# Kernel optimization log

Measured on AMD Instinct MI355X. Metric: run time of the kernel, lower is better.

Reference implementation:

```python
import jax, jax.numpy as jnp
import numpy as np

B, S, N, F, H, E, L = 16, 64, 128, 16, 64, 1024, 2
NEG_SLOPE = 0.2


def _gat_layer(h, src, tgt, Wl, bl, Wr, br, att, bo):
    # h: [B,S,N,H]; src/tgt: [Et] (edges incl. self-loops)
    xl = jnp.einsum('bsnf,hf->bsnh', h, Wl) + bl
    xr = jnp.einsum('bsnf,hf->bsnh', h, Wr) + br
    e = xl[:, :, src] + xr[:, :, tgt]                       # [B,S,Et,H]
    e = jnp.where(e > 0, e, NEG_SLOPE * e)                  # leaky_relu(0.2)
    a = jnp.einsum('bseh,h->bse', e, att)                   # [B,S,Et]
    # segment softmax over target node (stable)
    m = jnp.full(a.shape[:2] + (N,), -jnp.inf, a.dtype).at[:, :, tgt].max(a)
    p = jnp.exp(a - m[:, :, tgt])
    z = jnp.zeros(a.shape[:2] + (N,), a.dtype).at[:, :, tgt].add(p)
    alpha = p / z[:, :, tgt]
    out = jnp.zeros_like(xl).at[:, :, tgt].add(alpha[..., None] * xl[:, :, src])
    return out + bo


def _forward(x, edge_index, in_W, in_b, gat_Wl, gat_bl, gat_Wr, gat_br,
             gat_att, gat_bias, gru_Wih, gru_Whh, gru_bih, gru_bhh,
             oh_W1, oh_b1, oh_W2, oh_b2, dh_W1, dh_b1, dh_W2, dh_b2):
    ar = jnp.arange(N, dtype=edge_index.dtype)
    ei = jnp.concatenate([edge_index, jnp.stack([ar, ar])], axis=1)  # add self-loops
    src, tgt = ei[0], ei[1]
    h = jnp.einsum('bsnf,hf->bsnh', x, in_W) + in_b          # input_proj
    for l in range(L):
        h = jax.nn.relu(_gat_layer(h, src, tgt, gat_Wl[l], gat_bl[l],
                                   gat_Wr[l], gat_br[l], gat_att[l], gat_bias[l]))
    # [B,S,N,H] -> sequences [B*N, S, H]; GRU, keep last state
    seqs = h.transpose(0, 2, 1, 3).reshape(B * N, S, H)

    def step(hprev, xt):
        gi = xt @ gru_Wih.T + gru_bih
        gh = hprev @ gru_Whh.T + gru_bhh
        ir, iz, inn = jnp.split(gi, 3, axis=-1)
        hr, hz, hn = jnp.split(gh, 3, axis=-1)
        r = jax.nn.sigmoid(ir + hr)
        zz = jax.nn.sigmoid(iz + hz)
        n = jnp.tanh(inn + r * hn)
        hnew = (1 - zz) * n + zz * hprev
        return hnew, None

    h0 = jnp.zeros((B * N, H), h.dtype)
    h_last, _ = jax.lax.scan(step, h0, seqs.transpose(1, 0, 2))
    h_last = h_last.reshape(B, N, H)

    def head(hh, W1, b1, W2, b2):
        return jax.nn.relu(hh @ W1.T + b1) @ W2.T + b2

    order = head(h_last, oh_W1, oh_b1, oh_W2, oh_b2)        # [B,N,1]
    demand = head(h_last, dh_W1, dh_b1, dh_W2, dh_b2)       # [B,N,1]
    return order, demand


def setup_inputs() -> dict:
    key = jax.random.key(0)
    ks = jax.random.split(key, 16)
    def g(i, shp, s=0.05):
        return (jax.random.normal(ks[i], shp) * s).astype(jnp.float32)
    x = jax.random.normal(ks[0], (B, S, N, F), dtype=jnp.float32)
    src = jax.random.randint(ks[1], (E,), 0, N)
    off = jax.random.randint(ks[2], (E,), 1, N)
    edge_index = jnp.stack([src, (src + off) % N]).astype(jnp.int32)  # no self-loops
    zf = lambda shp: jnp.zeros(shp, jnp.float32)
    return dict(
        x=x, edge_index=edge_index,
        in_W=g(3, (H, F)), in_b=zf((H,)),
        gat_Wl=g(4, (L, H, H)), gat_bl=zf((L, H)),
        gat_Wr=g(5, (L, H, H)), gat_br=zf((L, H)),
        gat_att=g(6, (L, H), 0.1), gat_bias=zf((L, H)),
        gru_Wih=g(7, (3 * H, H)), gru_Whh=g(8, (3 * H, H)),
        gru_bih=zf((3 * H,)), gru_bhh=zf((3 * H,)),
        oh_W1=g(9, (H // 2, H)), oh_b1=zf((H // 2,)),
        oh_W2=g(10, (1, H // 2)), oh_b2=zf((1,)),
        dh_W1=g(11, (H // 2, H)), dh_b1=zf((H // 2,)),
        dh_W2=g(12, (1, H // 2)), dh_b2=zf((1,)),
    )


def reference(x, edge_index, in_W, in_b, gat_Wl, gat_bl, gat_Wr, gat_br,
              gat_att, gat_bias, gru_Wih, gru_Whh, gru_bih, gru_bhh,
              oh_W1, oh_b1, oh_W2, oh_b2, dh_W1, dh_b1, dh_W2, dh_b2):
    return _forward(x, edge_index, in_W, in_b, gat_Wl, gat_bl, gat_Wr, gat_br,
                    gat_att, gat_bias, gru_Wih, gru_Whh, gru_bih, gru_bhh,
                    oh_W1, oh_b1, oh_W2, oh_b2, dh_W1, dh_b1, dh_W2, dh_b2)
```

## Files before the change

### kernel.cpp

```cpp
#include <hip/hip_runtime.h>
#include <math.h>

#define BB 16
#define SS 64
#define NN 128
#define FF 16
#define HH 64
#define EE 1024
#define ET 1152
#define LLAYERS 2
#define XPAD 65
#define RT (BB * SS * NN)

__device__ __forceinline__ float readlane_f(float v, int k) {
  return __int_as_float(__builtin_amdgcn_readlane(__float_as_int(v), k));
}
__device__ __forceinline__ unsigned flipf(float f) {
  unsigned u = __float_as_uint(f);
  unsigned mask = (u & 0x80000000u) ? 0xFFFFFFFFu : 0x80000000u;
  return u ^ mask;
}
__device__ __forceinline__ float unflipf(unsigned u) {
  unsigned b = (u & 0x80000000u) ? (u ^ 0x80000000u) : ~u;
  return __uint_as_float(b);
}
__device__ __forceinline__ float sigmoidf_(float x) { return 1.f / (1.f + expf(-x)); }

__global__ void setup_csr_kernel(const int* __restrict__ ei,
                                 int* __restrict__ off,
                                 int* __restrict__ csrc,
                                 int* __restrict__ ctgt) {
  __shared__ int deg[NN], cur[NN], offs[NN + 1];
  int tid = threadIdx.x;
  if (tid < NN) deg[tid] = 0;
  __syncthreads();
  for (int e = tid; e < ET; e += 256) {
    int tg = (e < EE) ? ei[EE + e] : (e - EE);
    atomicAdd(&deg[tg], 1);
  }
  __syncthreads();
  if (tid == 0) {
    int s = 0;
    for (int i = 0; i < NN; ++i) { offs[i] = s; s += deg[i]; }
    offs[NN] = s;
  }
  __syncthreads();
  if (tid < NN) cur[tid] = offs[tid];
  if (tid <= NN) off[tid] = offs[tid];
  __syncthreads();
  for (int e = tid; e < ET; e += 256) {
    int sv, tg;
    if (e < EE) { sv = ei[e]; tg = ei[EE + e]; }
    else        { sv = e - EE; tg = e - EE; }
    int pos = atomicAdd(&cur[tg], 1);
    csrc[pos] = sv;
    ctgt[pos] = tg;
  }
}

__global__ __launch_bounds__(256) void input_proj_kernel(
    const float* __restrict__ x, const float* __restrict__ W,
    const float* __restrict__ bvec, float* __restrict__ h) {
  int lane = threadIdx.x & 63;
  int wid = threadIdx.x >> 6;
  float wreg[FF];
#pragma unroll
  for (int i = 0; i < FF / 4; ++i)
    *(float4*)&wreg[4 * i] = ((const float4*)(W + lane * FF))[i];
  float bias = bvec[lane];
  int row0 = __builtin_amdgcn_readfirstlane((blockIdx.x * 4 + wid) * 32);
#pragma unroll 2
  for (int r = 0; r < 32; ++r) {
    int row = row0 + r;
    const float* xr = x + row * FF;
    float acc = bias;
#pragma unroll
    for (int f = 0; f < FF; ++f) acc += xr[f] * wreg[f];
    h[row * HH + lane] = acc;
  }
}

__global__ __launch_bounds__(128) void xlxr_kernel(
    const float* __restrict__ hin,
    const float* __restrict__ Wl, const float* __restrict__ bl,
    const float* __restrict__ Wr, const float* __restrict__ br,
    float* __restrict__ xl, float* __restrict__ xr) {
  __shared__ float lsh[64 * 68];
  int tid = threadIdx.x;
  int j = tid & 63;
  int w = tid >> 6;
  int row0 = blockIdx.x * 64;
  {
    const float4* src4 = (const float4*)(hin + (size_t)row0 * HH);
#pragma unroll
    for (int i = 0; i < 8; ++i) {
      int idx = i * 128 + tid;
      int r = idx >> 4, c = idx & 15;
      *(float4*)&lsh[r * 68 + c * 4] = src4[idx];
    }
  }
  const float* W  = w ? Wr : Wl;
  const float* bv = w ? br : bl;
  float* outp     = w ? xr : xl;
  float wreg[HH];
  {
    const float4* ws_ = (const float4*)(W + (size_t)j * HH);
#pragma unroll
    for (int i = 0; i < HH / 4; ++i) *(float4*)&wreg[4 * i] = ws_[i];
  }
  float bias = bv[j];
  int rloc = j & 31;
  __syncthreads();

#pragma unroll 1
  for (int b = 0; b < 2; ++b) {
    float hreg[32];
    {
      const float* hr = &lsh[(b * 32 + rloc) * 68 + 32];
#pragma unroll
      for (int i = 0; i < 8; ++i)
        *(float4*)&hreg[4 * i] = *(const float4*)&hr[4 * i];
    }
#pragma unroll 1
    for (int r = 0; r < 32; ++r) {
      const float* hrow = &lsh[(b * 32 + r) * 68];
      float a0 = bias, a1 = 0.f, a2 = 0.f, a3 = 0.f;
#pragma unroll
      for (int k = 0; k < 32; k += 4) {
        float4 hb = *(const float4*)&hrow[k];
        a0 += hb.x * wreg[k + 0];
        a1 += hb.y * wreg[k + 1];
        a2 += hb.z * wreg[k + 2];
        a3 += hb.w * wreg[k + 3];
      }
#pragma unroll
      for (int q = 0; q < 32; q += 4) {
        a0 += readlane_f(hreg[q + 0], r) * wreg[32 + q + 0];
        a1 += readlane_f(hreg[q + 1], r) * wreg[32 + q + 1];
        a2 += readlane_f(hreg[q + 2], r) * wreg[32 + q + 2];
        a3 += readlane_f(hreg[q + 3], r) * wreg[32 + q + 3];
      }
      outp[(size_t)(row0 + b * 32 + r) * HH + j] = (a0 + a1) + (a2 + a3);
    }
  }
}

__global__ __launch_bounds__(256) void gat_edge_kernel(
    const float* __restrict__ xl_g, const float* __restrict__ xr_g,
    float* __restrict__ hout,
    const int* __restrict__ csr_off, const int* __restrict__ csr_src,
    const int* __restrict__ csr_tgt,
    const float* __restrict__ att, const float* __restrict__ bo) {
  __shared__ float xl_sh[NN * XPAD];
  __shared__ float xr_sh[NN * XPAD];
  __shared__ float p_sh[ET];
  __shared__ int st_sh[ET];
  __shared__ unsigned m_sh[NN];
  int tid = threadIdx.x, lane = tid & 63, wid = tid >> 6;
  int base = blockIdx.x * (NN * HH);

#pragma unroll 1
  for (int i = tid * 4; i < NN * HH; i += 256 * 4) {
    int row = i >> 6, h = i & 63;
    float4 vl = *(const float4*)(xl_g + base + i);
    float4 vr = *(const float4*)(xr_g + base + i);
    float* dl = xl_sh + row * XPAD + h;
    float* dr = xr_sh + row * XPAD + h;
    dl[0] = vl.x; dl[1] = vl.y; dl[2] = vl.z; dl[3] = vl.w;
    dr[0] = vr.x; dr[1] = vr.y; dr[2] = vr.z; dr[3] = vr.w;
  }
  for (int i = tid; i < ET; i += 256)
    st_sh[i] = csr_src[i] | (csr_tgt[i] << 16);
  if (tid < NN) m_sh[tid] = 0u;
  __syncthreads();

#pragma unroll 1
  for (int e = tid; e < ET; e += 256) {
    int st = st_sh[e];
    int s = st & 0xffff, tg = st >> 16;
    const float* xlr = xl_sh + s * XPAD;
    const float* xrr = xr_sh + tg * XPAD;
    float a0 = 0.f, a1 = 0.f, a2 = 0.f, a3 = 0.f;
#pragma unroll
    for (int h = 0; h < HH; h += 4) {
      float v0 = xlr[h + 0] + xrr[h + 0]; v0 = (v0 > 0.f) ? v0 : 0.2f * v0;
      float v1 = xlr[h + 1] + xrr[h + 1]; v1 = (v1 > 0.f) ? v1 : 0.2f * v1;
      float v2 = xlr[h + 2] + xrr[h + 2]; v2 = (v2 > 0.f) ? v2 : 0.2f * v2;
      float v3 = xlr[h + 3] + xrr[h + 3]; v3 = (v3 > 0.f) ? v3 : 0.2f * v3;
      a0 += v0 * att[h + 0];
      a1 += v1 * att[h + 1];
      a2 += v2 * att[h + 2];
      a3 += v3 * att[h + 3];
    }
    float a = (a0 + a1) + (a2 + a3);
    p_sh[e] = a;
    atomicMax(&m_sh[tg], flipf(a));
  }
  __syncthreads();

  for (int e = tid; e < ET; e += 256) {
    int tg = st_sh[e] >> 16;
    p_sh[e] = expf(p_sh[e] - unflipf(m_sh[tg]));
  }
  __syncthreads();

  float bo_l = bo[lane];
#pragma unroll 1
  for (int n = wid; n < NN; n += 4) {
    int o0 = __builtin_amdgcn_readfirstlane(csr_off[n]);
    int o1 = __builtin_amdgcn_readfirstlane(csr_off[n + 1]);
    float acc = 0.f, z = 0.f;
    for (int i = o0; i < o1; ++i) {
      float p = p_sh[i];
      int s = st_sh[i] & 0xffff;
      acc += p * xl_sh[s * XPAD + lane];
      z += p;
    }
    float o = acc / z + bo_l;
    hout[base + n * HH + lane] = fmaxf(o, 0.f);
  }
}

__device__ __forceinline__ void gemm_half(
    const float* __restrict__ hin, int base,
    const float* __restrict__ W, const float* __restrict__ bvec,
    float* __restrict__ out_sh, int half, int lane) {
  float wreg[HH];
#pragma unroll
  for (int i = 0; i < HH / 4; ++i)
    *(float4*)&wreg[4 * i] = ((const float4*)(W + lane * HH))[i];
  float bias = bvec[lane];
  int n0 = __builtin_amdgcn_readfirstlane(half * 64);
#pragma unroll 1
  for (int nd = 0; nd < 64; ++nd) {
    int node = n0 + nd;
    const float* hrow = hin + base + node * HH;
    float a0 = bias, a1 = 0.f, a2 = 0.f, a3 = 0.f;
#pragma unroll
    for (int f = 0; f < HH; f += 4) {
      a0 += hrow[f + 0] * wreg[f + 0];
      a1 += hrow[f + 1] * wreg[f + 1];
      a2 += hrow[f + 2] * wreg[f + 2];
      a3 += hrow[f + 3] * wreg[f + 3];
    }
    out_sh[node * HH + lane] = (a0 + a1) + (a2 + a3);
  }
}

__global__ __launch_bounds__(256) void gat_fused_kernel(
    const float* __restrict__ hin, float* __restrict__ hout,
    const int* __restrict__ csr_off, const int* __restrict__ csr_src,
    const int* __restrict__ csr_tgt,
    const float* __restrict__ Wl, const float* __restrict__ bl,
    const float* __restrict__ Wr, const float* __restrict__ br,
    const float* __restrict__ att, const float* __restrict__ bo) {
  __shared__ float xl_sh[NN * HH];
  __shared__ float xr_sh[NN * HH];
  __shared__ float p_sh[ET];
  __shared__ int st_sh[ET];
  __shared__ unsigned m_sh[NN];
  int tid = threadIdx.x, lane = tid & 63, wid = tid >> 6;
  int base = blockIdx.x * (NN * HH);

  for (int i = tid; i < ET; i += 256)
    st_sh[i] = csr_src[i] | (csr_tgt[i] << 16);
  if (tid < NN) m_sh[tid] = 0u;

  if (wid < 2) gemm_half(hin, base, Wl, bl, xl_sh, wid & 1, lane);
  else         gemm_half(hin, base, Wr, br, xr_sh, wid & 1, lane);

  float att_l = att[lane];
  float bo_l = bo[lane];
  __syncthreads();

#pragma unroll 1
  for (int e = wid; e < ET; e += 4) {
    int st = st_sh[e];
    int s = st & 0xffff, tg = st >> 16;
    float v = xl_sh[s * HH + lane] + xr_sh[tg * HH + lane];
    v = (v > 0.f) ? v : 0.2f * v;
    float prod = v * att_l;
#pragma unroll
    for (int mm = 32; mm; mm >>= 1) prod += __shfl_xor(prod, mm);
    if (lane == 0) {
      p_sh[e] = prod;
      atomicMax(&m_sh[tg], flipf(prod));
    }
  }
  __syncthreads();

  for (int e = tid; e < ET; e += 256) {
    int tg = st_sh[e] >> 16;
    p_sh[e] = expf(p_sh[e] - unflipf(m_sh[tg]));
  }
  __syncthreads();

#pragma unroll 1
  for (int n = wid; n < NN; n += 4) {
    int o0 = csr_off[n], o1 = csr_off[n + 1];
    float acc = 0.f, z = 0.f;
    for (int i = o0; i < o1; ++i) {
      float p = p_sh[i];
      int s = st_sh[i] & 0xffff;
      acc += p * xl_sh[s * HH + lane];
      z += p;
    }
    float o = acc / z + bo_l;
    hout[base + n * HH + lane] = fmaxf(o, 0.f);
  }
}

__global__ __launch_bounds__(192) void gi_proj_kernel(
    const float* __restrict__ hin, const float* __restrict__ Wih,
    const float* __restrict__ bih, float* __restrict__ gi) {
  __shared__ float lsh[64 * 68];
  int tid = threadIdx.x;
  int j = tid & 63;
  int g = tid >> 6;
  int row0 = blockIdx.x * 64;
  {
    const float4* src4 = (const float4*)(hin + (size_t)row0 * HH);
#pragma unroll 1
    for (int i = tid; i < 1024; i += 192) {
      int r = i >> 4, c = i & 15;
      *(float4*)&lsh[r * 68 + c * 4] = src4[i];
    }
  }
  float wreg[HH];
  {
    const float4* ws_ = (const float4*)(Wih + (size_t)(g * 64 + j) * HH);
#pragma unroll
    for (int i = 0; i < HH / 4; ++i) *(float4*)&wreg[4 * i] = ws_[i];
  }
  float bias = bih[g * 64 + j];
  int rloc = j & 31;
  __syncthreads();

#pragma unroll 1
  for (int b = 0; b < 2; ++b) {
    float hreg[32];
    {
      const float* hr = &lsh[(b * 32 + rloc) * 68 + 32];
#pragma unroll
      for (int i = 0; i < 8; ++i)
        *(float4*)&hreg[4 * i] = *(const float4*)&hr[4 * i];
    }
#pragma unroll 1
    for (int r = 0; r < 32; ++r) {
      const float* hrow = &lsh[(b * 32 + r) * 68];
      float a0 = bias, a1 = 0.f, a2 = 0.f, a3 = 0.f;
#pragma unroll
      for (int k = 0; k < 32; k += 4) {
        float4 hb = *(const float4*)&hrow[k];
        a0 += hb.x * wreg[k + 0];
        a1 += hb.y * wreg[k + 1];
        a2 += hb.z * wreg[k + 2];
        a3 += hb.w * wreg[k + 3];
      }
#pragma unroll
      for (int q = 0; q < 32; q += 4) {
        a0 += readlane_f(hreg[q + 0], r) * wreg[32 + q + 0];
        a1 += readlane_f(hreg[q + 1], r) * wreg[32 + q + 1];
        a2 += readlane_f(hreg[q + 2], r) * wreg[32 + q + 2];
        a3 += readlane_f(hreg[q + 3], r) * wreg[32 + q + 3];
      }
      gi[(size_t)(row0 + b * 32 + r) * 192 + g * 64 + j] = (a0 + a1) + (a2 + a3);
    }
  }
}

__global__ __launch_bounds__(64, 2) void gru_rec_kernel(
    const float* __restrict__ gi,
    const float* __restrict__ Whh, const float* __restrict__ bhh,
    const float* __restrict__ oW1, const float* __restrict__ ob1,
    const float* __restrict__ oW2, const float* __restrict__ ob2,
    const float* __restrict__ dW1, const float* __restrict__ db1,
    const float* __restrict__ dW2, const float* __restrict__ db2,
    float* __restrict__ out) {
  int lane = threadIdx.x;
  int seq = blockIdx.x;
  int b = seq >> 7, n = seq & (NN - 1);

  float wr[HH], wz[HH], wn[HH];
  {
    const float4* s0 = (const float4*)(Whh + (size_t)(0 * 64 + lane) * HH);
    const float4* s1 = (const float4*)(Whh + (size_t)(1 * 64 + lane) * HH);
    const float4* s2 = (const float4*)(Whh + (size_t)(2 * 64 + lane) * HH);
#pragma unroll
    for (int i = 0; i < HH / 4; ++i) {
      *(float4*)&wr[4 * i] = s0[i];
      *(float4*)&wz[4 * i] = s1[i];
      *(float4*)&wn[4 * i] = s2[i];
    }
  }
  float br_ = bhh[lane], bz_ = bhh[64 + lane], bn_ = bhh[128 + lane];

  const float* gbase = gi + ((size_t)b * SS * NN + (size_t)n) * 192;
  float gir = gbase[lane], giz = gbase[64 + lane], gin = gbase[128 + lane];
  const float* g1 = gbase + (size_t)NN * 192;
  float pir = g1[lane], piz = g1[64 + lane], pin = g1[128 + lane];
  float hj = 0.f;

#pragma unroll 1
  for (int t = 0; t < SS; ++t) {
    float qir = 0.f, qiz = 0.f, qin = 0.f;
    if (t + 2 < SS) {
      const float* g2 = gbase + (size_t)(t + 2) * NN * 192;
      qir = g2[lane]; qiz = g2[64 + lane]; qin = g2[128 + lane];
    }
    float ar0 = br_, ar1 = 0.f, az0 = bz_, az1 = 0.f, an0 = bn_, an1 = 0.f;
#pragma unroll
    for (int k = 0; k < HH; k += 2) {
      float h0 = readlane_f(hj, k), h1 = readlane_f(hj, k + 1);
      ar0 += h0 * wr[k];     az0 += h0 * wz[k];     an0 += h0 * wn[k];
      ar1 += h1 * wr[k + 1]; az1 += h1 * wz[k + 1]; an1 += h1 * wn[k + 1];
    }
    float r  = sigmoidf_(gir + ar0 + ar1);
    float z  = sigmoidf_(giz + az0 + az1);
    float nn_ = tanhf(gin + r * (an0 + an1));
    hj = (1.f - z) * nn_ + z * hj;
    gir = pir; giz = piz; gin = pin;
    pir = qir; piz = qiz; pin = qin;
  }

  int half = lane >> 5, jp = lane & 31;
  const float* W1 = half ? dW1 : oW1;
  const float* b1 = half ? db1 : ob1;
  const float* W2 = half ? dW2 : oW2;
  const float* b2 = half ? db2 : ob2;
  float wv[HH];
#pragma unroll
  for (int i = 0; i < HH / 4; ++i)
    *(float4*)&wv[4 * i] = ((const float4*)(W1 + jp * HH))[i];
  float acc = b1[jp];
#pragma unroll
  for (int k = 0; k < HH; ++k)
    acc += readlane_f(hj, k) * wv[k];
  float val = fmaxf(acc, 0.f) * W2[jp];
  val += __shfl_down(val, 16, 32);
  val += __shfl_down(val, 8, 32);
  val += __shfl_down(val, 4, 32);
  val += __shfl_down(val, 2, 32);
  val += __shfl_down(val, 1, 32);
  if (jp == 0) out[half * (BB * NN) + seq] = val + b2[0];
}

__global__ __launch_bounds__(192, 3) void gru_fused_kernel(
    const float* __restrict__ hbuf,
    const float* __restrict__ Wih, const float* __restrict__ Whh,
    const float* __restrict__ bih, const float* __restrict__ bhh,
    const float* __restrict__ oW1, const float* __restrict__ ob1,
    const float* __restrict__ oW2, const float* __restrict__ ob2,
    const float* __restrict__ dW1, const float* __restrict__ db1,
    const float* __restrict__ dW2, const float* __restrict__ db2,
    float* __restrict__ out) {
  __shared__ float gi_sh[SS * 3 * HH];
  __shared__ float exch[2][3][HH];

  int lane = threadIdx.x & 63;
  int g = (int)threadIdx.x >> 6;
  int seq = blockIdx.x;
  int b = seq >> 7, n = seq & (NN - 1);
  const float* xbase = hbuf + ((size_t)b * SS * NN + (size_t)n) * HH;

  {
    float w[HH];
    const float4* wsrc = (const float4*)(Wih + (size_t)(g * 64 + lane) * HH);
#pragma unroll
    for (int i = 0; i < HH / 4; ++i) *(float4*)&w[4 * i] = wsrc[i];
    float bias = bih[g * 64 + lane];
#pragma unroll 2
    for (int t = 0; t < SS; ++t) {
      const float* xr = xbase + (size_t)t * NN * HH;
      float a0 = bias, a1 = 0.f, a2 = 0.f, a3 = 0.f;
#pragma unroll
      for (int k = 0; k < HH; k += 4) {
        float4 xb = *(const float4*)(xr + k);
        a0 += xb.x * w[k + 0];
        a1 += xb.y * w[k + 1];
        a2 += xb.z * w[k + 2];
        a3 += xb.w * w[k + 3];
      }
      gi_sh[(t * 3 + g) * HH + lane] = (a0 + a1) + (a2 + a3);
    }
  }

  float whh[HH];
  {
    const float4* wsrc = (const float4*)(Whh + (size_t)(g * 64 + lane) * HH);
#pragma unroll
    for (int i = 0; i < HH / 4; ++i) *(float4*)&whh[4 * i] = wsrc[i];
  }
  float bhg = bhh[g * 64 + lane];
  float hj = 0.f;
  __syncthreads();

#pragma unroll 1
  for (int t = 0; t < SS; ++t) {
    float a0 = bhg, a1 = 0.f, a2 = 0.f, a3 = 0.f;
#pragma unroll
    for (int k = 0; k < HH; k += 4) {
      a0 += readlane_f(hj, k + 0) * whh[k + 0];
      a1 += readlane_f(hj, k + 1) * whh[k + 1];
      a2 += readlane_f(hj, k + 2) * whh[k + 2];
      a3 += readlane_f(hj, k + 3) * whh[k + 3];
    }
    float gh = (a0 + a1) + (a2 + a3);
    int slot = t & 1;
    exch[slot][g][lane] = gh;
    __syncthreads();
    float ghr = exch[slot][0][lane];
    float ghz = exch[slot][1][lane];
    float ghn = exch[slot][2][lane];
    float gir = gi_sh[(t * 3 + 0) * HH + lane];
    float giz = gi_sh[(t * 3 + 1) * HH + lane];
    float gin = gi_sh[(t * 3 + 2) * HH + lane];
    float r  = sigmoidf_(gir + ghr);
    float z  = sigmoidf_(giz + ghz);
    float nn_ = tanhf(gin + r * ghn);
    hj = (1.f - z) * nn_ + z * hj;
  }

  if (g == 0) {
    int half = lane >> 5, jp = lane & 31;
    const float* W1 = half ? dW1 : oW1;
    const float* b1 = half ? db1 : ob1;
    const float* W2 = half ? dW2 : oW2;
    const float* b2 = half ? db2 : ob2;
    float wv[HH];
#pragma unroll
    for (int i = 0; i < HH / 4; ++i)
      *(float4*)&wv[4 * i] = ((const float4*)(W1 + jp * HH))[i];
    float acc = b1[jp];
#pragma unroll
    for (int k = 0; k < HH; ++k)
      acc += readlane_f(hj, k) * wv[k];
    float val = fmaxf(acc, 0.f) * W2[jp];
    val += __shfl_down(val, 16, 32);
    val += __shfl_down(val, 8, 32);
    val += __shfl_down(val, 4, 32);
    val += __shfl_down(val, 2, 32);
    val += __shfl_down(val, 1, 32);
    if (jp == 0) out[half * (BB * NN) + seq] = val + b2[0];
  }
}

extern "C" void kernel_launch(void* const* d_in, const int* in_sizes, int n_in,
                              void* d_out, int out_size, void* d_ws, size_t ws_size,
                              hipStream_t stream) {
  const float* x       = (const float*)d_in[0];
  const int*   ei      = (const int*)d_in[1];
  const float* in_W    = (const float*)d_in[2];
  const float* in_b    = (const float*)d_in[3];
  const float* gat_Wl  = (const float*)d_in[4];
  const float* gat_bl  = (const float*)d_in[5];
  const float* gat_Wr  = (const float*)d_in[6];
  const float* gat_br  = (const float*)d_in[7];
  const float* gat_att = (const float*)d_in[8];
  const float* gat_bias= (const float*)d_in[9];
  const float* gru_Wih = (const float*)d_in[10];
  const float* gru_Whh = (const float*)d_in[11];
  const float* gru_bih = (const float*)d_in[12];
  const float* gru_bhh = (const float*)d_in[13];
  const float* oh_W1   = (const float*)d_in[14];
  const float* oh_b1   = (const float*)d_in[15];
  const float* oh_W2   = (const float*)d_in[16];
  const float* oh_b2   = (const float*)d_in[17];
  const float* dh_W1   = (const float*)d_in[18];
  const float* dh_b1   = (const float*)d_in[19];
  const float* dh_W2   = (const float*)d_in[20];
  const float* dh_b2   = (const float*)d_in[21];
  float* out = (float*)d_out;

  char* ws = (char*)d_ws;
  size_t hfloats = (size_t)BB * SS * NN * HH;
  float* hbuf = (float*)ws;
  size_t off_csr = hfloats * sizeof(float);
  size_t off_buf = off_csr + (160 + 2 * ET) * sizeof(int);
  off_buf = (off_buf + 255) & ~(size_t)255;
  int* csr_off = (int*)(ws + off_csr);
  int* csr_src = csr_off + 160;
  int* csr_tgt = csr_src + ET;
  float* xlbuf = (float*)(ws + off_buf);
  float* xrbuf = xlbuf + hfloats;
  size_t need_gat = off_buf + 2 * hfloats * sizeof(float);
  bool big_gat = (ws_size >= need_gat);
  float* gibuf = (float*)(ws + off_buf);
  size_t need_gru = off_buf + (size_t)RT * 192 * sizeof(float);
  bool big_gru = (ws_size >= need_gru);

  setup_csr_kernel<<<1, 256, 0, stream>>>(ei, csr_off, csr_src, csr_tgt);
  input_proj_kernel<<<(BB * SS * NN) / (4 * 32), 256, 0, stream>>>(x, in_W, in_b, hbuf);
  for (int l = 0; l < LLAYERS; ++l) {
    if (big_gat) {
      xlxr_kernel<<<RT / 64, 128, 0, stream>>>(
          hbuf, gat_Wl + l * HH * HH, gat_bl + l * HH,
          gat_Wr + l * HH * HH, gat_br + l * HH, xlbuf, xrbuf);
      gat_edge_kernel<<<BB * SS, 256, 0, stream>>>(
          xlbuf, xrbuf, hbuf, csr_off, csr_src, csr_tgt,
          gat_att + l * HH, gat_bias + l * HH);
    } else {
      gat_fused_kernel<<<BB * SS, 256, 0, stream>>>(
          hbuf, hbuf, csr_off, csr_src, csr_tgt,
          gat_Wl + l * HH * HH, gat_bl + l * HH,
          gat_Wr + l * HH * HH, gat_br + l * HH,
          gat_att + l * HH, gat_bias + l * HH);
    }
  }
  if (big_gru) {
    gi_proj_kernel<<<RT / 64, 192, 0, stream>>>(hbuf, gru_Wih, gru_bih, gibuf);
    gru_rec_kernel<<<BB * NN, 64, 0, stream>>>(
        gibuf, gru_Whh, gru_bhh,
        oh_W1, oh_b1, oh_W2, oh_b2, dh_W1, dh_b1, dh_W2, dh_b2, out);
  } else {
    gru_fused_kernel<<<BB * NN, 192, 0, stream>>>(
        hbuf, gru_Wih, gru_Whh, gru_bih, gru_bhh,
        oh_W1, oh_b1, oh_W2, oh_b2, dh_W1, dh_b1, dh_W2, dh_b2, out);
  }
}
```

Baseline: 632.1 us.

## Fuse GAT xl/xr projection into edge kernel with shared-memory staging

Replaces the separate xl/xr projection kernel and edge-softmax kernel with one 512-thread kernel per (batch, step) slice. The h slice is staged in LDS, the projections are computed straight into LDS, and then the attention and aggregation run from there. This removes the global write and read of the xl/xr buffers, which are twice the size of h, plus one launch per layer. The cost is a heavier LDS footprint per block, which may limit occupancy. The old fallback path for a small workspace is also removed.

```diff
diff --git a/kernel.cpp b/kernel.cpp
--- a/kernel.cpp
+++ b/kernel.cpp
@@ -10,6 +10,7 @@
 #define ET 1152
 #define LLAYERS 2
 #define XPAD 65
+#define HSTRIDE 68
 #define RT (BB * SS * NN)
 
 __device__ __forceinline__ float readlane_f(float v, int k) {
@@ -80,50 +81,59 @@
   }
 }
 
-__global__ __launch_bounds__(128) void xlxr_kernel(
-    const float* __restrict__ hin,
+__global__ __launch_bounds__(512) void gat_fused2_kernel(
+    float* __restrict__ hio,
+    const int* __restrict__ csr_off, const int* __restrict__ csr_src,
+    const int* __restrict__ csr_tgt,
     const float* __restrict__ Wl, const float* __restrict__ bl,
     const float* __restrict__ Wr, const float* __restrict__ br,
-    float* __restrict__ xl, float* __restrict__ xr) {
-  __shared__ float lsh[64 * 68];
-  int tid = threadIdx.x;
-  int j = tid & 63;
-  int w = tid >> 6;
-  int row0 = blockIdx.x * 64;
-  {
-    const float4* src4 = (const float4*)(hin + (size_t)row0 * HH);
-#pragma unroll
-    for (int i = 0; i < 8; ++i) {
-      int idx = i * 128 + tid;
+    const float* __restrict__ att, const float* __restrict__ bo) {
+  __shared__ float h_sh[NN * HSTRIDE];
+  __shared__ float xl_sh[NN * XPAD];
+  __shared__ float xr_sh[NN * XPAD];
+  __shared__ float p_sh[ET];
+  __shared__ int st_sh[ET];
+  __shared__ unsigned m_sh[NN];
+  int tid = threadIdx.x, lane = tid & 63, wid = tid >> 6;
+  int base = blockIdx.x * (NN * HH);
+
+  {
+    const float4* src4 = (const float4*)(hio + base);
+#pragma unroll
+    for (int i = 0; i < 4; ++i) {
+      int idx = i * 512 + tid;
       int r = idx >> 4, c = idx & 15;
-      *(float4*)&lsh[r * 68 + c * 4] = src4[idx];
-    }
-  }
-  const float* W  = w ? Wr : Wl;
-  const float* bv = w ? br : bl;
-  float* outp     = w ? xr : xl;
-  float wreg[HH];
-  {
-    const float4* ws_ = (const float4*)(W + (size_t)j * HH);
-#pragma unroll
-    for (int i = 0; i < HH / 4; ++i) *(float4*)&wreg[4 * i] = ws_[i];
-  }
-  float bias = bv[j];
-  int rloc = j & 31;
-  __syncthreads();
-
-#pragma unroll 1
-  for (int b = 0; b < 2; ++b) {
+      *(float4*)&h_sh[r * HSTRIDE + c * 4] = src4[idx];
+    }
+  }
+  for (int i = tid; i < ET; i += 512)
+    st_sh[i] = csr_src[i] | (csr_tgt[i] << 16);
+  if (tid < NN) m_sh[tid] = 0u;
+  __syncthreads();
+
+  {
+    int mat = wid >> 2;
+    const float* W  = mat ? Wr : Wl;
+    const float* bv = mat ? br : bl;
+    float* outsh    = mat ? xr_sh : xl_sh;
+    float wreg[HH];
+    {
+      const float4* ws_ = (const float4*)(W + (size_t)lane * HH);
+#pragma unroll
+      for (int i = 0; i < HH / 4; ++i) *(float4*)&wreg[4 * i] = ws_[i];
+    }
+    float bias = bv[lane];
+    int r0 = (wid & 3) * 32;
     float hreg[32];
     {
-      const float* hr = &lsh[(b * 32 + rloc) * 68 + 32];
+      const float* hr = &h_sh[(r0 + (lane & 31)) * HSTRIDE + 32];
 #pragma unroll
       for (int i = 0; i < 8; ++i)
         *(float4*)&hreg[4 * i] = *(const float4*)&hr[4 * i];
     }
 #pragma unroll 1
     for (int r = 0; r < 32; ++r) {
-      const float* hrow = &lsh[(b * 32 + r) * 68];
+      const float* hrow = &h_sh[(r0 + r) * HSTRIDE];
       float a0 = bias, a1 = 0.f, a2 = 0.f, a3 = 0.f;
 #pragma unroll
       for (int k = 0; k < 32; k += 4) {
@@ -140,42 +150,13 @@
         a2 += readlane_f(hreg[q + 2], r) * wreg[32 + q + 2];
         a3 += readlane_f(hreg[q + 3], r) * wreg[32 + q + 3];
       }
-      outp[(size_t)(row0 + b * 32 + r) * HH + j] = (a0 + a1) + (a2 + a3);
-    }
-  }
-}
-
-__global__ __launch_bounds__(256) void gat_edge_kernel(
-    const float* __restrict__ xl_g, const float* __restrict__ xr_g,
-    float* __restrict__ hout,
-    const int* __restrict__ csr_off, const int* __restrict__ csr_src,
-    const int* __restrict__ csr_tgt,
-    const float* __restrict__ att, const float* __restrict__ bo) {
-  __shared__ float xl_sh[NN * XPAD];
-  __shared__ float xr_sh[NN * XPAD];
-  __shared__ float p_sh[ET];
-  __shared__ int st_sh[ET];
-  __shared__ unsigned m_sh[NN];
-  int tid = threadIdx.x, lane = tid & 63, wid = tid >> 6;
-  int base = blockIdx.x * (NN * HH);
-
-#pragma unroll 1
-  for (int i = tid * 4; i < NN * HH; i += 256 * 4) {
-    int row = i >> 6, h = i & 63;
-    float4 vl = *(const float4*)(xl_g + base + i);
-    float4 vr = *(const float4*)(xr_g + base + i);
-    float* dl = xl_sh + row * XPAD + h;
-    float* dr = xr_sh + row * XPAD + h;
-    dl[0] = vl.x; dl[1] = vl.y; dl[2] = vl.z; dl[3] = vl.w;
-    dr[0] = vr.x; dr[1] = vr.y; dr[2] = vr.z; dr[3] = vr.w;
-  }
-  for (int i = tid; i < ET; i += 256)
-    st_sh[i] = csr_src[i] | (csr_tgt[i] << 16);
-  if (tid < NN) m_sh[tid] = 0u;
-  __syncthreads();
-
-#pragma unroll 1
-  for (int e = tid; e < ET; e += 256) {
+      outsh[(r0 + r) * XPAD + lane] = (a0 + a1) + (a2 + a3);
+    }
+  }
+  __syncthreads();
+
+#pragma unroll 1
+  for (int e = tid; e < ET; e += 512) {
     int st = st_sh[e];
     int s = st & 0xffff, tg = st >> 16;
     const float* xlr = xl_sh + s * XPAD;
@@ -198,7 +179,7 @@
   }
   __syncthreads();
 
-  for (int e = tid; e < ET; e += 256) {
+  for (int e = tid; e < ET; e += 512) {
     int tg = st_sh[e] >> 16;
     p_sh[e] = expf(p_sh[e] - unflipf(m_sh[tg]));
   }
@@ -206,7 +187,7 @@
 
   float bo_l = bo[lane];
 #pragma unroll 1
-  for (int n = wid; n < NN; n += 4) {
+  for (int n = wid; n < NN; n += 8) {
     int o0 = __builtin_amdgcn_readfirstlane(csr_off[n]);
     int o1 = __builtin_amdgcn_readfirstlane(csr_off[n + 1]);
     float acc = 0.f, z = 0.f;
@@ -217,96 +198,7 @@
       z += p;
     }
     float o = acc / z + bo_l;
-    hout[base + n * HH + lane] = fmaxf(o, 0.f);
-  }
-}
-
-__device__ __forceinline__ void gemm_half(
-    const float* __restrict__ hin, int base,
-    const float* __restrict__ W, const float* __restrict__ bvec,
-    float* __restrict__ out_sh, int half, int lane) {
-  float wreg[HH];
-#pragma unroll
-  for (int i = 0; i < HH / 4; ++i)
-    *(float4*)&wreg[4 * i] = ((const float4*)(W + lane * HH))[i];
-  float bias = bvec[lane];
-  int n0 = __builtin_amdgcn_readfirstlane(half * 64);
-#pragma unroll 1
-  for (int nd = 0; nd < 64; ++nd) {
-    int node = n0 + nd;
-    const float* hrow = hin + base + node * HH;
-    float a0 = bias, a1 = 0.f, a2 = 0.f, a3 = 0.f;
-#pragma unroll
-    for (int f = 0; f < HH; f += 4) {
-      a0 += hrow[f + 0] * wreg[f + 0];
-      a1 += hrow[f + 1] * wreg[f + 1];
-      a2 += hrow[f + 2] * wreg[f + 2];
-      a3 += hrow[f + 3] * wreg[f + 3];
-    }
-    out_sh[node * HH + lane] = (a0 + a1) + (a2 + a3);
-  }
-}
-
-__global__ __launch_bounds__(256) void gat_fused_kernel(
-    const float* __restrict__ hin, float* __restrict__ hout,
-    const int* __restrict__ csr_off, const int* __restrict__ csr_src,
-    const int* __restrict__ csr_tgt,
-    const float* __restrict__ Wl, const float* __restrict__ bl,
-    const float* __restrict__ Wr, const float* __restrict__ br,
-    const float* __restrict__ att, const float* __restrict__ bo) {
-  __shared__ float xl_sh[NN * HH];
-  __shared__ float xr_sh[NN * HH];
-  __shared__ float p_sh[ET];
-  __shared__ int st_sh[ET];
-  __shared__ unsigned m_sh[NN];
-  int tid = threadIdx.x, lane = tid & 63, wid = tid >> 6;
-  int base = blockIdx.x * (NN * HH);
-
-  for (int i = tid; i < ET; i += 256)
-    st_sh[i] = csr_src[i] | (csr_tgt[i] << 16);
-  if (tid < NN) m_sh[tid] = 0u;
-
-  if (wid < 2) gemm_half(hin, base, Wl, bl, xl_sh, wid & 1, lane);
-  else         gemm_half(hin, base, Wr, br, xr_sh, wid & 1, lane);
-
-  float att_l = att[lane];
-  float bo_l = bo[lane];
-  __syncthreads();
-
-#pragma unroll 1
-  for (int e = wid; e < ET; e += 4) {
-    int st = st_sh[e];
-    int s = st & 0xffff, tg = st >> 16;
-    float v = xl_sh[s * HH + lane] + xr_sh[tg * HH + lane];
-    v = (v > 0.f) ? v : 0.2f * v;
-    float prod = v * att_l;
-#pragma unroll
-    for (int mm = 32; mm; mm >>= 1) prod += __shfl_xor(prod, mm);
-    if (lane == 0) {
-      p_sh[e] = prod;
-      atomicMax(&m_sh[tg], flipf(prod));
-    }
-  }
-  __syncthreads();
-
-  for (int e = tid; e < ET; e += 256) {
-    int tg = st_sh[e] >> 16;
-    p_sh[e] = expf(p_sh[e] - unflipf(m_sh[tg]));
-  }
-  __syncthreads();
-
-#pragma unroll 1
-  for (int n = wid; n < NN; n += 4) {
-    int o0 = csr_off[n], o1 = csr_off[n + 1];
-    float acc = 0.f, z = 0.f;
-    for (int i = o0; i < o1; ++i) {
-      float p = p_sh[i];
-      int s = st_sh[i] & 0xffff;
-      acc += p * xl_sh[s * HH + lane];
-      z += p;
-    }
-    float o = acc / z + bo_l;
-    hout[base + n * HH + lane] = fmaxf(o, 0.f);
+    hio[base + n * HH + lane] = fmaxf(o, 0.f);
   }
 }
 
@@ -581,10 +473,6 @@
   int* csr_off = (int*)(ws + off_csr);
   int* csr_src = csr_off + 160;
   int* csr_tgt = csr_src + ET;
-  float* xlbuf = (float*)(ws + off_buf);
-  float* xrbuf = xlbuf + hfloats;
-  size_t need_gat = off_buf + 2 * hfloats * sizeof(float);
-  bool big_gat = (ws_size >= need_gat);
   float* gibuf = (float*)(ws + off_buf);
   size_t need_gru = off_buf + (size_t)RT * 192 * sizeof(float);
   bool big_gru = (ws_size >= need_gru);
@@ -592,20 +480,11 @@
   setup_csr_kernel<<<1, 256, 0, stream>>>(ei, csr_off, csr_src, csr_tgt);
   input_proj_kernel<<<(BB * SS * NN) / (4 * 32), 256, 0, stream>>>(x, in_W, in_b, hbuf);
   for (int l = 0; l < LLAYERS; ++l) {
-    if (big_gat) {
-      xlxr_kernel<<<RT / 64, 128, 0, stream>>>(
-          hbuf, gat_Wl + l * HH * HH, gat_bl + l * HH,
-          gat_Wr + l * HH * HH, gat_br + l * HH, xlbuf, xrbuf);
-      gat_edge_kernel<<<BB * SS, 256, 0, stream>>>(
-          xlbuf, xrbuf, hbuf, csr_off, csr_src, csr_tgt,
-          gat_att + l * HH, gat_bias + l * HH);
-    } else {
-      gat_fused_kernel<<<BB * SS, 256, 0, stream>>>(
-          hbuf, hbuf, csr_off, csr_src, csr_tgt,
-          gat_Wl + l * HH * HH, gat_bl + l * HH,
-          gat_Wr + l * HH * HH, gat_br + l * HH,
-          gat_att + l * HH, gat_bias + l * HH);
-    }
+    gat_fused2_kernel<<<BB * SS, 512, 0, stream>>>(
+        hbuf, csr_off, csr_src, csr_tgt,
+        gat_Wl + l * HH * HH, gat_bl + l * HH,
+        gat_Wr + l * HH * HH, gat_br + l * HH,
+        gat_att + l * HH, gat_bias + l * HH);
   }
   if (big_gru) {
     gi_proj_kernel<<<RT / 64, 192, 0, stream>>>(hbuf, gru_Wih, gru_bih, gibuf);
```

Measured after the change: 630.8 us. About the same (-0.2%).
